# Performance work log

Measured on AMD Instinct MI355X. Metric: run time of the kernel, lower is better.

## Reference

```python
import jax, jax.numpy as jnp
from jax import lax
import numpy as np
import math

D_STATE = 2
D_CONV = 4

def _ln(x, g, b, eps=1e-5):
    m = x.mean(-1, keepdims=True)
    v = ((x - m) ** 2).mean(-1, keepdims=True)
    return (x - m) * lax.rsqrt(v + eps) * g + b

def _mamba(x, Win, convw, convb, Wx, Wdt, bdt, Alog, Dp, Wout):
    # x: (b, L, d_model); expand=1 so d_inner == d_model
    b, L, dm = x.shape
    di = Win.shape[0] // 2
    n = Alog.shape[1]
    dtr = Wdt.shape[1]
    k = convw.shape[-1]
    xz = x @ Win.T                                   # (b, L, 2*di)
    xi, z = xz[..., :di], xz[..., di:]
    # causal depthwise conv1d along the sequence axis (pad left k-1, truncate to L)
    xc = jnp.pad(xi, ((0, 0), (k - 1, 0), (0, 0))).transpose(0, 2, 1)  # (b, di, L+k-1)
    xc = lax.conv_general_dilated(xc, convw, (1,), 'VALID',
                                  dimension_numbers=('NCH', 'OIH', 'NCH'),
                                  feature_group_count=di)
    xi = jax.nn.silu(xc.transpose(0, 2, 1) + convb)  # (b, L, di)
    dbl = xi @ Wx.T                                  # (b, L, dtr + 2n)
    dt = jax.nn.softplus(dbl[..., :dtr] @ Wdt.T + bdt)   # (b, L, di)
    Bm = dbl[..., dtr:dtr + n]                       # (b, L, n)
    Cm = dbl[..., dtr + n:]                          # (b, L, n)
    A = -jnp.exp(Alog)                               # (di, n)
    dA = jnp.exp(dt[..., None] * A)                  # (b, L, di, n)
    dBx = dt[..., None] * Bm[:, :, None, :] * xi[..., None]  # (b, L, di, n)

    def step(h, inp):
        dA_t, dBx_t, C_t = inp
        h = dA_t * h + dBx_t                         # (b, di, n)
        return h, jnp.einsum('bdn,bn->bd', h, C_t)

    h0 = jnp.zeros((b, di, n), x.dtype)
    _, ys = lax.scan(step, h0, (dA.transpose(1, 0, 2, 3),
                                dBx.transpose(1, 0, 2, 3),
                                Cm.transpose(1, 0, 2)))
    y = ys.transpose(1, 0, 2) + Dp * xi              # (b, L, di)
    y = y * jax.nn.silu(z)
    return y @ Wout.T                                # (b, L, out_c)

def setup_inputs():
    key = jax.random.key(0)
    ks = jax.random.split(key, 32)
    B, C, H, W = 16, 256, 32, 32
    dm = H * W
    di = dm                      # expand = 1
    dtr = math.ceil(dm / 16)     # dt_rank = 64
    n, k = D_STATE, D_CONV

    def rn(i, shape, s):
        return (jax.random.normal(ks[i], shape) * s).astype(jnp.float32)

    inp = {'x': rn(0, (B, C, H, W), 1.0)}

    def mamba_p(pfx, base):
        inp[pfx + 'Win'] = rn(base, (2 * di, dm), dm ** -0.5)
        inp[pfx + 'convw'] = rn(base + 1, (di, 1, k), k ** -0.5)
        inp[pfx + 'convb'] = jnp.zeros((di,), jnp.float32)
        inp[pfx + 'Wx'] = rn(base + 2, (dtr + 2 * n, di), di ** -0.5)
        inp[pfx + 'Wdt'] = rn(base + 3, (di, dtr), dtr ** -0.5)
        inp[pfx + 'bdt'] = rn(base + 4, (di,), 0.1)
        inp[pfx + 'Alog'] = jnp.log(jnp.broadcast_to(
            jnp.arange(1, n + 1, dtype=jnp.float32), (di, n)))
        inp[pfx + 'D'] = jnp.ones((di,), jnp.float32)
        inp[pfx + 'Wout'] = rn(base + 5, (dm, di), di ** -0.5)  # out_c = sp_dim2^2 = dm

    mamba_p('m1_', 1)
    mamba_p('m2_', 8)
    inp['ln1_g'] = jnp.ones((dm,), jnp.float32)
    inp['ln1_b'] = jnp.zeros((dm,), jnp.float32)
    inp['ln2_g'] = jnp.ones((dm,), jnp.float32)
    inp['ln2_b'] = jnp.zeros((dm,), jnp.float32)
    inp['W_mid'] = rn(15, (C, C), C ** -0.5)   # Linear_Layer inside LIFM_SPA (bias=False)
    inp['W_spa'] = rn(16, (dm, dm), dm ** -0.5)  # linear_spa (nn.Linear default bias)
    inp['b_spa'] = jnp.zeros((dm,), jnp.float32)
    inp['W_res'] = rn(17, (C, C), C ** -0.5)   # lin_chan in residual path (bias=False)
    return inp

def reference(x, m1_Win, m1_convw, m1_convb, m1_Wx, m1_Wdt, m1_bdt, m1_Alog, m1_D, m1_Wout,
              m2_Win, m2_convw, m2_convb, m2_Wx, m2_Wdt, m2_bdt, m2_Alog, m2_D, m2_Wout,
              ln1_g, ln1_b, ln2_g, ln2_b, W_mid, W_spa, b_spa, W_res):
    b, c, h, w = x.shape
    hw = h * w
    # LIFM_SPA path: SSM_spa -> Linear_Layer (channel mix + SiLU) -> SSM_spa
    s = _mamba(x.reshape(b, c, hw), m1_Win, m1_convw, m1_convb,
               m1_Wx, m1_Wdt, m1_bdt, m1_Alog, m1_D, m1_Wout)
    s = _ln(s, ln1_g, ln1_b)                               # (b, c, hw)
    s = jax.nn.silu(jnp.einsum('bcs,oc->bos', s, W_mid))   # channel linear, SiLU (dropout off in eval)
    s = _mamba(s, m2_Win, m2_convw, m2_convb,
               m2_Wx, m2_Wdt, m2_bdt, m2_Alog, m2_D, m2_Wout)
    s = _ln(s, ln2_g, ln2_b)                               # (b, out_c, hw)
    # residual path: spatial linear (+bias) + SiLU, then channel linear + SiLU
    r = jax.nn.silu(x.reshape(b, c, hw) @ W_spa.T + b_spa)
    r = jax.nn.silu(jnp.einsum('bcs,oc->bos', r, W_res))
    return jax.nn.silu(s + r).reshape(b, -1, h, w)
```

## Files before the change

kernel.cpp:

```cpp
#include <hip/hip_runtime.h>
#include <math.h>

#define BATCH 16
#define LSEQ  256
#define DM    1024
#define DI    1024
#define NROWS (BATCH*LSEQ)
#define DTR   64
#define TWO_DI 2048
#define NCH   16
#define CHL   16

typedef __attribute__((ext_vector_type(8))) short short8;
typedef __attribute__((ext_vector_type(4))) float floatx4;

__device__ __forceinline__ float siluf(float x) {
    return x / (1.0f + __expf(-x));
}
__device__ __forceinline__ float softplusf(float x) {
    return fmaxf(x, 0.0f) + log1pf(__expf(-fabsf(x)));
}
__device__ __forceinline__ unsigned short f2bf(float f) {
    unsigned int u = __float_as_uint(f);
    u += 0x7fffu + ((u >> 16) & 1u);
    return (unsigned short)(u >> 16);
}
__device__ __forceinline__ float bf2f(unsigned short s) {
    return __uint_as_float(((unsigned int)s) << 16);
}
__device__ __forceinline__ void async16(const short* g, short* l) {
    __builtin_amdgcn_global_load_lds(
        (const __attribute__((address_space(1))) unsigned int*)g,
        (__attribute__((address_space(3))) unsigned int*)l,
        16, 0, 0);
}

__global__ __launch_bounds__(256) void cast_bf16(
    const float* __restrict__ in, unsigned short* __restrict__ out)
{
    const size_t i = ((size_t)blockIdx.x * 256 + threadIdx.x) * 4;
    const float4 v = *(const float4*)(in + i);
    union { unsigned short s[4]; unsigned long long u; } p;
    p.s[0] = f2bf(v.x); p.s[1] = f2bf(v.y);
    p.s[2] = f2bf(v.z); p.s[3] = f2bf(v.w);
    *(unsigned long long*)(out + i) = p.u;
}

template <int EP, int OUT16>
__global__ __launch_bounds__(256) void gemm_bf16_nt(
    const short* __restrict__ A,
    const short* __restrict__ W,
    const float* __restrict__ bias,
    void* __restrict__ Cout,
    int M, int N, int K)
{
    __shared__ short As[128 * 32];
    __shared__ short Bs[128 * 32];

    const int tid  = threadIdx.x;
    const int wave = tid >> 6;
    const int lane = tid & 63;
    const int wm = wave >> 1;
    const int wn = wave & 1;
    const int row0 = blockIdx.y * 128;
    const int col0 = blockIdx.x * 128;

    const int srow  = lane >> 2;
    const int skoff = (lane & 3) * 8;
    const short* gA0 = A + (size_t)(row0 + wave * 32 + srow) * K + skoff;
    const short* gA1 = gA0 + (size_t)16 * K;
    const short* gB0 = W + (size_t)(col0 + wave * 32 + srow) * K + skoff;
    const short* gB1 = gB0 + (size_t)16 * K;
    short* lA0 = As + (wave * 32) * 32;
    short* lA1 = lA0 + 16 * 32;
    short* lB0 = Bs + (wave * 32) * 32;
    short* lB1 = lB0 + 16 * 32;

    const int fr = lane & 15;
    const int fk = (lane >> 4) * 8;

    floatx4 acc[4][4] = {};

    for (int k0 = 0; k0 < K; k0 += 32) {
        async16(gA0 + k0, lA0);
        async16(gA1 + k0, lA1);
        async16(gB0 + k0, lB0);
        async16(gB1 + k0, lB1);
        __syncthreads();

        short8 af[4], bfr[4];
        #pragma unroll
        for (int t = 0; t < 4; t++) {
            af[t]  = *(const short8*)&As[(wm * 64 + t * 16 + fr) * 32 + fk];
            bfr[t] = *(const short8*)&Bs[(wn * 64 + t * 16 + fr) * 32 + fk];
        }
        #pragma unroll
        for (int i = 0; i < 4; i++)
            #pragma unroll
            for (int j = 0; j < 4; j++)
                acc[i][j] = __builtin_amdgcn_mfma_f32_16x16x32_bf16(
                    af[i], bfr[j], acc[i][j], 0, 0, 0);
        __syncthreads();
    }

    const int crow = row0 + wm * 64 + (lane >> 4) * 4;
    const int ccol = col0 + wn * 64 + (lane & 15);
    #pragma unroll
    for (int i = 0; i < 4; i++) {
        #pragma unroll
        for (int j = 0; j < 4; j++) {
            const int c = ccol + j * 16;
            #pragma unroll
            for (int r = 0; r < 4; r++) {
                float v = acc[i][j][r];
                if (EP == 1) v = softplusf(v + bias[c]);
                else if (EP == 2) v = siluf(v + bias[c]);
                const size_t idx = (size_t)(crow + i * 16 + r) * N + c;
                if (OUT16) ((unsigned short*)Cout)[idx] = f2bf(v);
                else       ((float*)Cout)[idx] = v;
            }
        }
    }
}

template <int OUT16>
__global__ __launch_bounds__(256) void gemm_bf16_bat(
    const short* __restrict__ A,
    const short* __restrict__ Wb,
    void* __restrict__ Cout,
    int M, int N, int K)
{
    const int bz = blockIdx.z;
    const short* W = Wb + (size_t)bz * N * K;

    __shared__ short As[128 * 32];
    __shared__ short Bs[128 * 32];

    const int tid  = threadIdx.x;
    const int wave = tid >> 6;
    const int lane = tid & 63;
    const int wm = wave >> 1;
    const int wn = wave & 1;
    const int row0 = blockIdx.y * 128;
    const int col0 = blockIdx.x * 128;

    const int srow  = lane >> 2;
    const int skoff = (lane & 3) * 8;
    const short* gA0 = A + (size_t)(row0 + wave * 32 + srow) * K + skoff;
    const short* gA1 = gA0 + (size_t)16 * K;
    const short* gB0 = W + (size_t)(col0 + wave * 32 + srow) * K + skoff;
    const short* gB1 = gB0 + (size_t)16 * K;
    short* lA0 = As + (wave * 32) * 32;
    short* lA1 = lA0 + 16 * 32;
    short* lB0 = Bs + (wave * 32) * 32;
    short* lB1 = lB0 + 16 * 32;

    const int fr = lane & 15;
    const int fk = (lane >> 4) * 8;

    floatx4 acc[4][4] = {};

    for (int k0 = 0; k0 < K; k0 += 32) {
        async16(gA0 + k0, lA0);
        async16(gA1 + k0, lA1);
        async16(gB0 + k0, lB0);
        async16(gB1 + k0, lB1);
        __syncthreads();

        short8 af[4], bfr[4];
        #pragma unroll
        for (int t = 0; t < 4; t++) {
            af[t]  = *(const short8*)&As[(wm * 64 + t * 16 + fr) * 32 + fk];
            bfr[t] = *(const short8*)&Bs[(wn * 64 + t * 16 + fr) * 32 + fk];
        }
        #pragma unroll
        for (int i = 0; i < 4; i++)
            #pragma unroll
            for (int j = 0; j < 4; j++)
                acc[i][j] = __builtin_amdgcn_mfma_f32_16x16x32_bf16(
                    af[i], bfr[j], acc[i][j], 0, 0, 0);
        __syncthreads();
    }

    const int crow = row0 + wm * 64 + (lane >> 4) * 4;
    const int ccol = col0 + wn * 64 + (lane & 15);
    #pragma unroll
    for (int i = 0; i < 4; i++) {
        #pragma unroll
        for (int j = 0; j < 4; j++) {
            const int c = ccol + j * 16;
            #pragma unroll
            for (int r = 0; r < 4; r++) {
                const float v = siluf(acc[i][j][r]);
                const size_t idx = (size_t)bz * M * N + (size_t)(crow + i * 16 + r) * N + c;
                if (OUT16) ((unsigned short*)Cout)[idx] = f2bf(v);
                else       ((float*)Cout)[idx] = v;
            }
        }
    }
}

__global__ __launch_bounds__(256) void gemm_nn_wcomb(
    const float* __restrict__ Wdt,
    const float* __restrict__ Wx,
    unsigned short* __restrict__ C16)
{
    __shared__ float Asf[16][64];
    __shared__ float Bsf[16][64];

    const int tid = threadIdx.x;
    const int tx = tid & 15;
    const int ty = tid >> 4;
    const int row0 = blockIdx.y * 64;
    const int col0 = blockIdx.x * 64;
    const int lrow = tid >> 2;
    const int lcol = (tid & 3) * 4;
    const int bk = tid >> 4;
    const int bn = (tid & 15) * 4;

    float acc[4][4] = {};

    for (int k0 = 0; k0 < 64; k0 += 16) {
        const float4 av = *(const float4*)(Wdt + (size_t)(row0 + lrow) * 64 + k0 + lcol);
        Asf[lcol + 0][lrow] = av.x;
        Asf[lcol + 1][lrow] = av.y;
        Asf[lcol + 2][lrow] = av.z;
        Asf[lcol + 3][lrow] = av.w;
        *(float4*)&Bsf[bk][bn] = *(const float4*)(Wx + (size_t)(k0 + bk) * 1024 + col0 + bn);
        __syncthreads();

        #pragma unroll
        for (int kk = 0; kk < 16; kk++) {
            const float4 a = *(const float4*)&Asf[kk][ty * 4];
            const float4 b = *(const float4*)&Bsf[kk][tx * 4];
            const float af[4] = {a.x, a.y, a.z, a.w};
            const float bfv[4] = {b.x, b.y, b.z, b.w};
            #pragma unroll
            for (int i = 0; i < 4; i++)
                #pragma unroll
                for (int j = 0; j < 4; j++)
                    acc[i][j] = fmaf(af[i], bfv[j], acc[i][j]);
        }
        __syncthreads();
    }

    #pragma unroll
    for (int i = 0; i < 4; i++) {
        const int r = row0 + ty * 4 + i;
        #pragma unroll
        for (int j = 0; j < 4; j++)
            C16[(size_t)r * 1024 + col0 + tx * 4 + j] = f2bf(acc[i][j]);
    }
}

__global__ __launch_bounds__(256) void conv_silu_bc(
    const float* __restrict__ xz,
    const float* __restrict__ convw,
    const float* __restrict__ convb,
    const float* __restrict__ Wx,
    unsigned short* __restrict__ xi16,
    float* __restrict__ bc)
{
    __shared__ float redc[4][4];
    const int r = blockIdx.x;
    const int l = r & (LSEQ - 1);
    const int tid = threadIdx.x;
    float p0 = 0.f, p1 = 0.f, p2 = 0.f, p3 = 0.f;
    #pragma unroll
    for (int i = 0; i < 4; i++) {
        const int d = tid + i * 256;
        const float w0 = convw[d * 4 + 0];
        const float w1 = convw[d * 4 + 1];
        const float w2 = convw[d * 4 + 2];
        const float w3 = convw[d * 4 + 3];
        float acc = w3 * xz[(size_t)r * TWO_DI + d];
        if (l >= 1) acc = fmaf(w2, xz[(size_t)(r - 1) * TWO_DI + d], acc);
        if (l >= 2) acc = fmaf(w1, xz[(size_t)(r - 2) * TWO_DI + d], acc);
        if (l >= 3) acc = fmaf(w0, xz[(size_t)(r - 3) * TWO_DI + d], acc);
        const float v = siluf(acc + convb[d]);
        xi16[(size_t)r * DI + d] = f2bf(v);
        p0 = fmaf(v, Wx[64 * 1024 + d], p0);
        p1 = fmaf(v, Wx[65 * 1024 + d], p1);
        p2 = fmaf(v, Wx[66 * 1024 + d], p2);
        p3 = fmaf(v, Wx[67 * 1024 + d], p3);
    }
    #pragma unroll
    for (int o = 32; o; o >>= 1) {
        p0 += __shfl_down(p0, o, 64);
        p1 += __shfl_down(p1, o, 64);
        p2 += __shfl_down(p2, o, 64);
        p3 += __shfl_down(p3, o, 64);
    }
    const int w = tid >> 6, lane = tid & 63;
    if (lane == 0) {
        redc[w][0] = p0; redc[w][1] = p1; redc[w][2] = p2; redc[w][3] = p3;
    }
    __syncthreads();
    if (tid < 4)
        bc[r * 4 + tid] = redc[0][tid] + redc[1][tid] + redc[2][tid] + redc[3][tid];
}

__global__ __launch_bounds__(256) void scan_part1(
    const unsigned short* __restrict__ dt16,
    const unsigned short* __restrict__ xi16,
    const float* __restrict__ bc,
    const float* __restrict__ Alog,
    float4* __restrict__ hc)
{
    const int d  = blockIdx.x * 256 + threadIdx.x;
    const int b  = blockIdx.y;
    const int ch = blockIdx.z;
    const float A0 = -__expf(Alog[d * 2 + 0]);
    const float A1 = -__expf(Alog[d * 2 + 1]);
    float h0 = 0.f, h1 = 0.f, p0 = 1.f, p1 = 1.f;
    const int r0 = b * LSEQ + ch * CHL;
    #pragma unroll 4
    for (int l = 0; l < CHL; l++) {
        const int r = r0 + l;
        const float dtv = bf2f(dt16[(size_t)r * DI + d]);
        const float xiv = bf2f(xi16[(size_t)r * DI + d]);
        const float4 bcv = *(const float4*)(bc + r * 4);
        const float e0 = __expf(dtv * A0);
        const float e1 = __expf(dtv * A1);
        const float dbx = dtv * xiv;
        h0 = fmaf(e0, h0, dbx * bcv.x);
        h1 = fmaf(e1, h1, dbx * bcv.y);
        p0 *= e0; p1 *= e1;
    }
    hc[(size_t)(b * NCH + ch) * DI + d] = make_float4(h0, h1, p0, p1);
}

__global__ __launch_bounds__(256) void scan_carry(
    const float4* __restrict__ hc,
    float2* __restrict__ ci)
{
    const int d = blockIdx.x * 256 + threadIdx.x;
    const int b = blockIdx.y;
    float c0 = 0.f, c1 = 0.f;
    #pragma unroll
    for (int ch = 0; ch < NCH; ch++) {
        const size_t idx = (size_t)(b * NCH + ch) * DI + d;
        const float4 v = hc[idx];
        ci[idx] = make_float2(c0, c1);
        c0 = fmaf(v.z, c0, v.x);
        c1 = fmaf(v.w, c1, v.y);
    }
}

__global__ __launch_bounds__(256) void scan_part2(
    const unsigned short* __restrict__ dt16,
    const unsigned short* __restrict__ xi16,
    const float* __restrict__ xz,
    const float* __restrict__ bc,
    const float* __restrict__ Alog,
    const float* __restrict__ Dp,
    const float2* __restrict__ ci,
    unsigned short* __restrict__ yg16)
{
    const int d  = blockIdx.x * 256 + threadIdx.x;
    const int b  = blockIdx.y;
    const int ch = blockIdx.z;
    const float A0 = -__expf(Alog[d * 2 + 0]);
    const float A1 = -__expf(Alog[d * 2 + 1]);
    const float Dv = Dp[d];
    const float2 c = ci[(size_t)(b * NCH + ch) * DI + d];
    float h0 = c.x, h1 = c.y;
    const int r0 = b * LSEQ + ch * CHL;
    #pragma unroll 4
    for (int l = 0; l < CHL; l++) {
        const int r = r0 + l;
        const float dtv = bf2f(dt16[(size_t)r * DI + d]);
        const float xiv = bf2f(xi16[(size_t)r * DI + d]);
        const float4 bcv = *(const float4*)(bc + r * 4);
        const float zv = xz[(size_t)r * TWO_DI + DI + d];
        const float e0 = __expf(dtv * A0);
        const float e1 = __expf(dtv * A1);
        const float dbx = dtv * xiv;
        h0 = fmaf(e0, h0, dbx * bcv.x);
        h1 = fmaf(e1, h1, dbx * bcv.y);
        const float y = fmaf(h0, bcv.z, fmaf(h1, bcv.w, Dv * xiv));
        yg16[(size_t)r * DI + d] = f2bf(y * siluf(zv));
    }
}

__global__ __launch_bounds__(256) void ln_kernel(
    float* __restrict__ s,
    const float* __restrict__ g,
    const float* __restrict__ bb)
{
    __shared__ float red[8];
    const size_t base = (size_t)blockIdx.x * DM;
    const int t = threadIdx.x;
    float x0 = s[base + t];
    float x1 = s[base + t + 256];
    float x2 = s[base + t + 512];
    float x3 = s[base + t + 768];
    float sum = x0 + x1 + x2 + x3;
    #pragma unroll
    for (int o = 32; o; o >>= 1) sum += __shfl_down(sum, o, 64);
    const int w = t >> 6, lane = t & 63;
    if (lane == 0) red[w] = sum;
    __syncthreads();
    const float m = (red[0] + red[1] + red[2] + red[3]) * (1.0f / 1024.0f);
    const float d0 = x0 - m, d1 = x1 - m, d2 = x2 - m, d3 = x3 - m;
    float ss = d0 * d0 + d1 * d1 + d2 * d2 + d3 * d3;
    #pragma unroll
    for (int o = 32; o; o >>= 1) ss += __shfl_down(ss, o, 64);
    if (lane == 0) red[4 + w] = ss;
    __syncthreads();
    const float var = (red[4] + red[5] + red[6] + red[7]) * (1.0f / 1024.0f);
    const float inv = rsqrtf(var + 1e-5f);
    s[base + t]       = d0 * inv * g[t]       + bb[t];
    s[base + t + 256] = d1 * inv * g[t + 256] + bb[t + 256];
    s[base + t + 512] = d2 * inv * g[t + 512] + bb[t + 512];
    s[base + t + 768] = d3 * inv * g[t + 768] + bb[t + 768];
}

__global__ __launch_bounds__(256) void transpose_cast(
    const float* __restrict__ in, unsigned short* __restrict__ out)
{
    __shared__ float tile[32][33];
    const int b = blockIdx.z;
    const int c0 = blockIdx.y * 32;
    const int s0 = blockIdx.x * 32;
    const int tx = threadIdx.x & 31;
    const int ty = threadIdx.x >> 5;
    const size_t ib = (size_t)b * 256 * 1024;
    const size_t ob = (size_t)b * 1024 * 256;
    #pragma unroll
    for (int i = 0; i < 4; i++)
        tile[tx][ty + i * 8] = in[ib + (size_t)(c0 + ty + i * 8) * 1024 + s0 + tx];
    __syncthreads();
    #pragma unroll
    for (int i = 0; i < 4; i++)
        out[ob + (size_t)(s0 + ty + i * 8) * 256 + c0 + tx] = f2bf(tile[ty + i * 8][tx]);
}

__global__ __launch_bounds__(256) void final_silu(
    const float* __restrict__ s, float* __restrict__ out)
{
    const size_t i = (size_t)blockIdx.x * 256 + threadIdx.x;
    out[i] = siluf(s[i] + out[i]);
}

extern "C" void kernel_launch(void* const* d_in, const int* in_sizes, int n_in,
                              void* d_out, int out_size, void* d_ws, size_t ws_size,
                              hipStream_t stream)
{
    const float* x        = (const float*)d_in[0];
    const float* m1_Win   = (const float*)d_in[1];
    const float* m1_convw = (const float*)d_in[2];
    const float* m1_convb = (const float*)d_in[3];
    const float* m1_Wx    = (const float*)d_in[4];
    const float* m1_Wdt   = (const float*)d_in[5];
    const float* m1_bdt   = (const float*)d_in[6];
    const float* m1_Alog  = (const float*)d_in[7];
    const float* m1_D     = (const float*)d_in[8];
    const float* m1_Wout  = (const float*)d_in[9];
    const float* m2_Win   = (const float*)d_in[10];
    const float* m2_convw = (const float*)d_in[11];
    const float* m2_convb = (const float*)d_in[12];
    const float* m2_Wx    = (const float*)d_in[13];
    const float* m2_Wdt   = (const float*)d_in[14];
    const float* m2_bdt   = (const float*)d_in[15];
    const float* m2_Alog  = (const float*)d_in[16];
    const float* m2_D     = (const float*)d_in[17];
    const float* m2_Wout  = (const float*)d_in[18];
    const float* ln1_g    = (const float*)d_in[19];
    const float* ln1_b    = (const float*)d_in[20];
    const float* ln2_g    = (const float*)d_in[21];
    const float* ln2_b    = (const float*)d_in[22];
    const float* W_mid    = (const float*)d_in[23];
    const float* W_spa    = (const float*)d_in[24];
    const float* b_spa    = (const float*)d_in[25];
    const float* W_res    = (const float*)d_in[26];

    float* ws = (float*)d_ws;
    size_t off = 0;
    float* buf_xz  = ws + off; off += (size_t)NROWS * TWO_DI;
    float* buf_s   = ws + off; off += (size_t)NROWS * DI;
    float* buf_bc  = ws + off; off += (size_t)NROWS * 4;
    float4* buf_hc = (float4*)(ws + off); off += (size_t)BATCH * NCH * DI * 4;
    float2* buf_ci = (float2*)(ws + off); off += (size_t)BATCH * NCH * DI * 2;
    unsigned short* bx     = (unsigned short*)(ws + off); off += (size_t)NROWS * DI / 2;
    unsigned short* xi16   = (unsigned short*)(ws + off); off += (size_t)NROWS * DI / 2;
    unsigned short* yg16   = (unsigned short*)(ws + off); off += (size_t)NROWS * DI / 2;
    unsigned short* sT16   = (unsigned short*)(ws + off); off += (size_t)NROWS * DI / 2;
    unsigned short* dt16   = (unsigned short*)(ws + off); off += (size_t)NROWS * DI / 2;
    unsigned short* win16  = (unsigned short*)(ws + off); off += (size_t)TWO_DI * DM / 2;
    unsigned short* wout16 = (unsigned short*)(ws + off); off += (size_t)DM * DI / 2;
    unsigned short* wspa16 = (unsigned short*)(ws + off); off += (size_t)DM * DM / 2;
    unsigned short* wcomb16= (unsigned short*)(ws + off); off += (size_t)DI * DI / 2;
    unsigned short* wmid16 = (unsigned short*)(ws + off); off += (size_t)LSEQ * LSEQ / 2;
    unsigned short* wres16 = (unsigned short*)(ws + off); off += (size_t)LSEQ * LSEQ / 2;
    unsigned short* t16 = yg16;
    float* buf_res = buf_xz;
    unsigned short* rT16 = sT16;
    (void)ws_size; (void)n_in; (void)in_sizes; (void)out_size;

    const dim3 blk(256);

    auto mamba = [&](const unsigned short* inp16, const float* Win,
                     const float* convw, const float* convb, const float* Wx,
                     const float* Wdt, const float* bdt, const float* Alog,
                     const float* Dp, const float* Wout, float* out_buf) {
        cast_bf16<<<dim3((TWO_DI * DM) / 1024), blk, 0, stream>>>(Win, win16);
        cast_bf16<<<dim3((DM * DI) / 1024), blk, 0, stream>>>(Wout, wout16);
        gemm_nn_wcomb<<<dim3(16, 16), blk, 0, stream>>>(Wdt, Wx, wcomb16);
        gemm_bf16_nt<0, 0><<<dim3(TWO_DI / 128, NROWS / 128), blk, 0, stream>>>(
            (const short*)inp16, (const short*)win16, nullptr, buf_xz,
            NROWS, TWO_DI, DM);
        conv_silu_bc<<<dim3(NROWS), blk, 0, stream>>>(
            buf_xz, convw, convb, Wx, xi16, buf_bc);
        gemm_bf16_nt<1, 1><<<dim3(DI / 128, NROWS / 128), blk, 0, stream>>>(
            (const short*)xi16, (const short*)wcomb16, bdt, dt16,
            NROWS, DI, DI);
        scan_part1<<<dim3(DI / 256, BATCH, NCH), blk, 0, stream>>>(
            dt16, xi16, buf_bc, Alog, buf_hc);
        scan_carry<<<dim3(DI / 256, BATCH), blk, 0, stream>>>(buf_hc, buf_ci);
        scan_part2<<<dim3(DI / 256, BATCH, NCH), blk, 0, stream>>>(
            dt16, xi16, buf_xz, buf_bc, Alog, Dp, buf_ci, yg16);
        gemm_bf16_nt<0, 0><<<dim3(DM / 128, NROWS / 128), blk, 0, stream>>>(
            (const short*)yg16, (const short*)wout16, nullptr, out_buf,
            NROWS, DM, DI);
    };

    cast_bf16<<<dim3((NROWS * DM) / 1024), blk, 0, stream>>>(x, bx);
    cast_bf16<<<dim3((DM * DM) / 1024), blk, 0, stream>>>(W_spa, wspa16);
    cast_bf16<<<dim3((LSEQ * LSEQ) / 1024), blk, 0, stream>>>(W_mid, wmid16);
    cast_bf16<<<dim3((LSEQ * LSEQ) / 1024), blk, 0, stream>>>(W_res, wres16);

    mamba(bx, m1_Win, m1_convw, m1_convb, m1_Wx, m1_Wdt, m1_bdt, m1_Alog, m1_D,
          m1_Wout, buf_s);
    ln_kernel<<<dim3(NROWS), blk, 0, stream>>>(buf_s, ln1_g, ln1_b);

    transpose_cast<<<dim3(32, 8, BATCH), blk, 0, stream>>>(buf_s, sT16);
    gemm_bf16_bat<1><<<dim3(DM / 128, LSEQ / 128, BATCH), blk, 0, stream>>>(
        (const short*)wmid16, (const short*)sT16, (void*)t16, LSEQ, DM, LSEQ);

    mamba(t16, m2_Win, m2_convw, m2_convb, m2_Wx, m2_Wdt, m2_bdt, m2_Alog,
          m2_D, m2_Wout, buf_s);
    ln_kernel<<<dim3(NROWS), blk, 0, stream>>>(buf_s, ln2_g, ln2_b);

    gemm_bf16_nt<2, 0><<<dim3(DM / 128, NROWS / 128), blk, 0, stream>>>(
        (const short*)bx, (const short*)wspa16, b_spa, buf_res,
        NROWS, DM, DM);
    transpose_cast<<<dim3(32, 8, BATCH), blk, 0, stream>>>(buf_res, rT16);
    gemm_bf16_bat<0><<<dim3(DM / 128, LSEQ / 128, BATCH), blk, 0, stream>>>(
        (const short*)wres16, (const short*)rT16, d_out, LSEQ, DM, LSEQ);

    final_silu<<<dim3((NROWS * DM) / 256), blk, 0, stream>>>(
        buf_s, (float*)d_out);
}
```

Measured before the change: 531.8 us.

## Double-buffer LDS in bf16 GEMM, shrink M tile to 64, merge batched variant

```diff
diff --git a/kernel.cpp b/kernel.cpp
--- a/kernel.cpp
+++ b/kernel.cpp
@@ -46,7 +46,7 @@
     *(unsigned long long*)(out + i) = p.u;
 }
 
-template <int EP, int OUT16>
+template <int EP, int OUT16, int BATW>
 __global__ __launch_bounds__(256) void gemm_bf16_nt(
     const short* __restrict__ A,
     const short* __restrict__ W,
@@ -54,59 +54,73 @@
     void* __restrict__ Cout,
     int M, int N, int K)
 {
-    __shared__ short As[128 * 32];
-    __shared__ short Bs[128 * 32];
+    __shared__ short As[2 * 64 * 32];
+    __shared__ short Bs[2 * 128 * 32];
+
+    const int bz = BATW ? blockIdx.z : 0;
+    const short* Wb = W + (size_t)bz * N * K;
+    const size_t cbase = (size_t)bz * M * N;
 
     const int tid  = threadIdx.x;
     const int wave = tid >> 6;
     const int lane = tid & 63;
     const int wm = wave >> 1;
     const int wn = wave & 1;
-    const int row0 = blockIdx.y * 128;
+    const int row0 = blockIdx.y * 64;
     const int col0 = blockIdx.x * 128;
 
-    const int srow  = lane >> 2;
-    const int skoff = (lane & 3) * 8;
-    const short* gA0 = A + (size_t)(row0 + wave * 32 + srow) * K + skoff;
-    const short* gA1 = gA0 + (size_t)16 * K;
-    const short* gB0 = W + (size_t)(col0 + wave * 32 + srow) * K + skoff;
-    const short* gB1 = gB0 + (size_t)16 * K;
-    short* lA0 = As + (wave * 32) * 32;
-    short* lA1 = lA0 + 16 * 32;
-    short* lB0 = Bs + (wave * 32) * 32;
-    short* lB1 = lB0 + 16 * 32;
+    const int srow  = tid >> 2;
+    const int skoff = (tid & 3) * 8;
+    const short* gA  = A  + (size_t)(row0 + srow) * K + skoff;
+    const short* gB0 = Wb + (size_t)(col0 + srow) * K + skoff;
+    const short* gB1 = Wb + (size_t)(col0 + 64 + srow) * K + skoff;
+    short* lA  = As + srow * 32 + skoff;
+    short* lB0 = Bs + srow * 32 + skoff;
+    short* lB1 = lB0 + 64 * 32;
 
     const int fr = lane & 15;
     const int fk = (lane >> 4) * 8;
 
-    floatx4 acc[4][4] = {};
-
+    floatx4 acc[2][4] = {};
+
+    async16(gA, lA);
+    async16(gB0, lB0);
+    async16(gB1, lB1);
+    __syncthreads();
+
+    int cur = 0;
     for (int k0 = 0; k0 < K; k0 += 32) {
-        async16(gA0 + k0, lA0);
-        async16(gA1 + k0, lA1);
-        async16(gB0 + k0, lB0);
-        async16(gB1 + k0, lB1);
-        __syncthreads();
-
-        short8 af[4], bfr[4];
-        #pragma unroll
-        for (int t = 0; t < 4; t++) {
-            af[t]  = *(const short8*)&As[(wm * 64 + t * 16 + fr) * 32 + fk];
-            bfr[t] = *(const short8*)&Bs[(wn * 64 + t * 16 + fr) * 32 + fk];
+        short8 af[2], bfr[4];
+        const short* Ac = As + cur * 64 * 32;
+        const short* Bc = Bs + cur * 128 * 32;
+        #pragma unroll
+        for (int i = 0; i < 2; i++)
+            af[i] = *(const short8*)&Ac[(wm * 32 + i * 16 + fr) * 32 + fk];
+        #pragma unroll
+        for (int j = 0; j < 4; j++)
+            bfr[j] = *(const short8*)&Bc[(wn * 64 + j * 16 + fr) * 32 + fk];
+
+        if (k0 + 32 < K) {
+            const int nb = (cur ^ 1);
+            async16(gA + k0 + 32,  lA  + nb * 64 * 32);
+            async16(gB0 + k0 + 32, lB0 + nb * 128 * 32);
+            async16(gB1 + k0 + 32, lB1 + nb * 128 * 32);
         }
-        #pragma unroll
-        for (int i = 0; i < 4; i++)
+
+        #pragma unroll
+        for (int i = 0; i < 2; i++)
             #pragma unroll
             for (int j = 0; j < 4; j++)
                 acc[i][j] = __builtin_amdgcn_mfma_f32_16x16x32_bf16(
                     af[i], bfr[j], acc[i][j], 0, 0, 0);
         __syncthreads();
-    }
-
-    const int crow = row0 + wm * 64 + (lane >> 4) * 4;
+        cur ^= 1;
+    }
+
+    const int crow = row0 + wm * 32 + (lane >> 4) * 4;
     const int ccol = col0 + wn * 64 + (lane & 15);
     #pragma unroll
-    for (int i = 0; i < 4; i++) {
+    for (int i = 0; i < 2; i++) {
         #pragma unroll
         for (int j = 0; j < 4; j++) {
             const int c = ccol + j * 16;
@@ -115,84 +129,8 @@
                 float v = acc[i][j][r];
                 if (EP == 1) v = softplusf(v + bias[c]);
                 else if (EP == 2) v = siluf(v + bias[c]);
-                const size_t idx = (size_t)(crow + i * 16 + r) * N + c;
-                if (OUT16) ((unsigned short*)Cout)[idx] = f2bf(v);
-                else       ((float*)Cout)[idx] = v;
-            }
-        }
-    }
-}
-
-template <int OUT16>
-__global__ __launch_bounds__(256) void gemm_bf16_bat(
-    const short* __restrict__ A,
-    const short* __restrict__ Wb,
-    void* __restrict__ Cout,
-    int M, int N, int K)
-{
-    const int bz = blockIdx.z;
-    const short* W = Wb + (size_t)bz * N * K;
-
-    __shared__ short As[128 * 32];
-    __shared__ short Bs[128 * 32];
-
-    const int tid  = threadIdx.x;
-    const int wave = tid >> 6;
-    const int lane = tid & 63;
-    const int wm = wave >> 1;
-    const int wn = wave & 1;
-    const int row0 = blockIdx.y * 128;
-    const int col0 = blockIdx.x * 128;
-
-    const int srow  = lane >> 2;
-    const int skoff = (lane & 3) * 8;
-    const short* gA0 = A + (size_t)(row0 + wave * 32 + srow) * K + skoff;
-    const short* gA1 = gA0 + (size_t)16 * K;
-    const short* gB0 = W + (size_t)(col0 + wave * 32 + srow) * K + skoff;
-    const short* gB1 = gB0 + (size_t)16 * K;
-    short* lA0 = As + (wave * 32) * 32;
-    short* lA1 = lA0 + 16 * 32;
-    short* lB0 = Bs + (wave * 32) * 32;
-    short* lB1 = lB0 + 16 * 32;
-
-    const int fr = lane & 15;
-    const int fk = (lane >> 4) * 8;
-
-    floatx4 acc[4][4] = {};
-
-    for (int k0 = 0; k0 < K; k0 += 32) {
-        async16(gA0 + k0, lA0);
-        async16(gA1 + k0, lA1);
-        async16(gB0 + k0, lB0);
-        async16(gB1 + k0, lB1);
-        __syncthreads();
-
-        short8 af[4], bfr[4];
-        #pragma unroll
-        for (int t = 0; t < 4; t++) {
-            af[t]  = *(const short8*)&As[(wm * 64 + t * 16 + fr) * 32 + fk];
-            bfr[t] = *(const short8*)&Bs[(wn * 64 + t * 16 + fr) * 32 + fk];
-        }
-        #pragma unroll
-        for (int i = 0; i < 4; i++)
-            #pragma unroll
-            for (int j = 0; j < 4; j++)
-                acc[i][j] = __builtin_amdgcn_mfma_f32_16x16x32_bf16(
-                    af[i], bfr[j], acc[i][j], 0, 0, 0);
-        __syncthreads();
-    }
-
-    const int crow = row0 + wm * 64 + (lane >> 4) * 4;
-    const int ccol = col0 + wn * 64 + (lane & 15);
-    #pragma unroll
-    for (int i = 0; i < 4; i++) {
-        #pragma unroll
-        for (int j = 0; j < 4; j++) {
-            const int c = ccol + j * 16;
-            #pragma unroll
-            for (int r = 0; r < 4; r++) {
-                const float v = siluf(acc[i][j][r]);
-                const size_t idx = (size_t)bz * M * N + (size_t)(crow + i * 16 + r) * N + c;
+                else if (EP == 3) v = siluf(v);
+                const size_t idx = cbase + (size_t)(crow + i * 16 + r) * N + c;
                 if (OUT16) ((unsigned short*)Cout)[idx] = f2bf(v);
                 else       ((float*)Cout)[idx] = v;
             }
@@ -507,12 +445,12 @@
         cast_bf16<<<dim3((TWO_DI * DM) / 1024), blk, 0, stream>>>(Win, win16);
         cast_bf16<<<dim3((DM * DI) / 1024), blk, 0, stream>>>(Wout, wout16);
         gemm_nn_wcomb<<<dim3(16, 16), blk, 0, stream>>>(Wdt, Wx, wcomb16);
-        gemm_bf16_nt<0, 0><<<dim3(TWO_DI / 128, NROWS / 128), blk, 0, stream>>>(
+        gemm_bf16_nt<0, 0, 0><<<dim3(TWO_DI / 128, NROWS / 64), blk, 0, stream>>>(
             (const short*)inp16, (const short*)win16, nullptr, buf_xz,
             NROWS, TWO_DI, DM);
         conv_silu_bc<<<dim3(NROWS), blk, 0, stream>>>(
             buf_xz, convw, convb, Wx, xi16, buf_bc);
-        gemm_bf16_nt<1, 1><<<dim3(DI / 128, NROWS / 128), blk, 0, stream>>>(
+        gemm_bf16_nt<1, 1, 0><<<dim3(DI / 128, NROWS / 64), blk, 0, stream>>>(
             (const short*)xi16, (const short*)wcomb16, bdt, dt16,
             NROWS, DI, DI);
         scan_part1<<<dim3(DI / 256, BATCH, NCH), blk, 0, stream>>>(
@@ -520,7 +458,7 @@
         scan_carry<<<dim3(DI / 256, BATCH), blk, 0, stream>>>(buf_hc, buf_ci);
         scan_part2<<<dim3(DI / 256, BATCH, NCH), blk, 0, stream>>>(
             dt16, xi16, buf_xz, buf_bc, Alog, Dp, buf_ci, yg16);
-        gemm_bf16_nt<0, 0><<<dim3(DM / 128, NROWS / 128), blk, 0, stream>>>(
+        gemm_bf16_nt<0, 0, 0><<<dim3(DM / 128, NROWS / 64), blk, 0, stream>>>(
             (const short*)yg16, (const short*)wout16, nullptr, out_buf,
             NROWS, DM, DI);
     };
@@ -535,19 +473,21 @@
     ln_kernel<<<dim3(NROWS), blk, 0, stream>>>(buf_s, ln1_g, ln1_b);
 
     transpose_cast<<<dim3(32, 8, BATCH), blk, 0, stream>>>(buf_s, sT16);
-    gemm_bf16_bat<1><<<dim3(DM / 128, LSEQ / 128, BATCH), blk, 0, stream>>>(
-        (const short*)wmid16, (const short*)sT16, (void*)t16, LSEQ, DM, LSEQ);
+    gemm_bf16_nt<3, 1, 1><<<dim3(DM / 128, LSEQ / 64, BATCH), blk, 0, stream>>>(
+        (const short*)wmid16, (const short*)sT16, nullptr, (void*)t16,
+        LSEQ, DM, LSEQ);
 
     mamba(t16, m2_Win, m2_convw, m2_convb, m2_Wx, m2_Wdt, m2_bdt, m2_Alog,
           m2_D, m2_Wout, buf_s);
     ln_kernel<<<dim3(NROWS), blk, 0, stream>>>(buf_s, ln2_g, ln2_b);
 
-    gemm_bf16_nt<2, 0><<<dim3(DM / 128, NROWS / 128), blk, 0, stream>>>(
+    gemm_bf16_nt<2, 0, 0><<<dim3(DM / 128, NROWS / 64), blk, 0, stream>>>(
         (const short*)bx, (const short*)wspa16, b_spa, buf_res,
         NROWS, DM, DM);
     transpose_cast<<<dim3(32, 8, BATCH), blk, 0, stream>>>(buf_res, rT16);
-    gemm_bf16_bat<0><<<dim3(DM / 128, LSEQ / 128, BATCH), blk, 0, stream>>>(
-        (const short*)wres16, (const short*)rT16, d_out, LSEQ, DM, LSEQ);
+    gemm_bf16_nt<3, 0, 1><<<dim3(DM / 128, LSEQ / 64, BATCH), blk, 0, stream>>>(
+        (const short*)wres16, (const short*)rT16, nullptr, d_out,
+        LSEQ, DM, LSEQ);
 
     final_silu<<<dim3((NROWS * DM) / 256), blk, 0, stream>>>(
         buf_s, (float*)d_out);
```

After: 459.7 us. -13.6%, faster.
